# Kernel optimization log

Measured on AMD Instinct MI355X. Metric: run time of the kernel, lower is better.

Reference implementation:

```python
import jax, jax.numpy as jnp
import numpy as np

K = 7          # kernel_size
PAD = K // 2   # padding


def _unfold(t):
    """im2col for kxk neighborhood: (B,C,H,W) -> (B,C,K*K,H,W), zero-padded."""
    B, C, H, W = t.shape
    p = jnp.pad(t, ((0, 0), (0, 0), (PAD, PAD), (PAD, PAD)))
    # row-major over kernel offsets matches F.unfold ordering
    wins = jnp.stack([p[:, :, i:i + H, j:j + W]
                      for i in range(K) for j in range(K)], axis=2)
    return wins


def setup_inputs() -> dict:
    key = jax.random.key(0)
    ks = jax.random.split(key, 7)
    B, C, H, W = 8, 128, 64, 64
    scale = 1.0 / np.sqrt(C)
    x = jax.random.normal(ks[0], (B, C, H, W), dtype=jnp.float32)
    Wq = jax.random.normal(ks[1], (C, C), dtype=jnp.float32) * scale
    Wk = jax.random.normal(ks[2], (C, C), dtype=jnp.float32) * scale
    Wv = jax.random.normal(ks[3], (C, C), dtype=jnp.float32) * scale
    bq = jax.random.normal(ks[4], (C,), dtype=jnp.float32) * 0.01
    bk = jax.random.normal(ks[5], (C,), dtype=jnp.float32) * 0.01
    bv = jax.random.normal(ks[6], (C,), dtype=jnp.float32) * 0.01
    return {"x": x, "Wq": Wq, "bq": bq, "Wk": Wk, "bk": bk, "Wv": Wv, "bv": bv}


def reference(x, Wq, bq, Wk, bk, Wv, bv):
    # 1x1 convs = channel GEMMs
    q = jnp.einsum('oc,bchw->bohw', Wq, x) + bq[:, None, None]
    k = jnp.einsum('oc,bchw->bohw', Wk, x) + bk[:, None, None]
    v = jnp.einsum('oc,bchw->bohw', Wv, x) + bv[:, None, None]
    k_unf = _unfold(k)   # (B,C,K*K,H,W)
    v_unf = _unfold(v)   # (B,C,K*K,H,W)
    # attention scores over the K*K neighborhood, summed over channels
    attn = jnp.einsum('bchw,bcphw->bphw', q, k_unf)
    attn = jax.nn.softmax(attn, axis=1)
    y = jnp.einsum('bphw,bcphw->bchw', attn, v_unf)
    return y
```

## Files before the change

### kernel.cpp

```cpp
#include <hip/hip_runtime.h>
#include <hip/hip_bf16.h>

#define CC   128
#define HH_  64
#define WW_  64
#define BB   8
#define HWSZ (HH_*WW_)
#define CHW  (CC*HWSZ)
#define BCHW (BB*CHW)
#define PAD  3
#define NP   49

typedef __attribute__((ext_vector_type(8))) short short8;
typedef __attribute__((ext_vector_type(4))) float float4v;

__global__ __launch_bounds__(256) void prep_w(
    const float* __restrict__ Wq, const float* __restrict__ Wk,
    const float* __restrict__ Wv,
    unsigned short* __restrict__ whi, unsigned short* __restrict__ wlo)
{
    int i = blockIdx.x * 256 + threadIdx.x;
    const float* src = (i < 16384) ? Wq : (i < 32768 ? Wk : Wv);
    float f = src[i & 16383];
    __hip_bfloat16 h = __float2bfloat16(f);
    float hf = __bfloat162float(h);
    __hip_bfloat16 l = __float2bfloat16(f - hf);
    unsigned short hu, lu;
    __builtin_memcpy(&hu, &h, 2);
    __builtin_memcpy(&lu, &l, 2);
    whi[i] = hu;
    wlo[i] = lu;
}

__global__ __launch_bounds__(256, 2) void qkv_mfma(
    const float* __restrict__ x,
    const unsigned short* __restrict__ whi, const unsigned short* __restrict__ wlo,
    const float* __restrict__ bq, const float* __restrict__ bk,
    const float* __restrict__ bv, float* __restrict__ qkv)
{
    __shared__ unsigned short xT[2][128][136];
    const int proj = blockIdx.y;
    const int n0g  = blockIdx.x << 7;
    const int b    = n0g >> 12;
    const int npx  = n0g & 4095;
    const int tid  = threadIdx.x;
    const int lane = tid & 63;
    const int wv   = tid >> 6;
    const int wm   = wv & 1, wn = wv >> 1;

    const float* xb = x + (size_t)b*CHW + npx;
    #pragma unroll
    for (int it = 0; it < 16; ++it) {
        int f  = tid + (it << 8);
        int c  = f >> 5;
        int p4 = (f & 31) << 2;
        float4 v = *(const float4*)&xb[(size_t)c*HWSZ + p4];
        float vv[4] = {v.x, v.y, v.z, v.w};
        #pragma unroll
        for (int u = 0; u < 4; ++u) {
            __hip_bfloat16 h = __float2bfloat16(vv[u]);
            float hf = __bfloat162float(h);
            __hip_bfloat16 l = __float2bfloat16(vv[u] - hf);
            unsigned short hu, lu;
            __builtin_memcpy(&hu, &h, 2);
            __builtin_memcpy(&lu, &l, 2);
            xT[0][p4 + u][c] = hu;
            xT[1][p4 + u][c] = lu;
        }
    }

    const float* Bp = (proj == 0) ? bq : (proj == 1 ? bk : bv);
    const int q4 = lane >> 4;
    float4v acc[4][4];
    #pragma unroll
    for (int sm = 0; sm < 4; ++sm) {
        const int mb = wm*64 + sm*16 + q4*4;
        float4v bi;
        bi[0] = Bp[mb+0]; bi[1] = Bp[mb+1]; bi[2] = Bp[mb+2]; bi[3] = Bp[mb+3];
        #pragma unroll
        for (int sn = 0; sn < 4; ++sn) acc[sm][sn] = bi;
    }

    __syncthreads();

    const unsigned short* Wh = whi + (size_t)proj*16384;
    const unsigned short* Wl = wlo + (size_t)proj*16384;
    const int kq8  = q4 << 3;
    const int mrow = lane & 15;

    for (int pass = 0; pass < 3; ++pass) {
        const unsigned short* Wp = (pass == 2) ? Wl : Wh;
        const int xi = (pass == 1) ? 1 : 0;
        #pragma unroll
        for (int kc = 0; kc < 4; ++kc) {
            const int kb = kc << 5;
            short8 a[4], bf[4];
            #pragma unroll
            for (int sm = 0; sm < 4; ++sm) {
                const int m = wm*64 + sm*16 + mrow;
                a[sm] = *(const short8*)&Wp[(size_t)m*CC + kb + kq8];
            }
            #pragma unroll
            for (int sn = 0; sn < 4; ++sn) {
                const int n = wn*64 + sn*16 + mrow;
                bf[sn] = *(const short8*)&xT[xi][n][kb + kq8];
            }
            #pragma unroll
            for (int sm = 0; sm < 4; ++sm)
                #pragma unroll
                for (int sn = 0; sn < 4; ++sn)
                    acc[sm][sn] = __builtin_amdgcn_mfma_f32_16x16x32_bf16(
                        a[sm], bf[sn], acc[sm][sn], 0, 0, 0);
        }
    }

    float* op = qkv + (size_t)proj*BCHW + (size_t)b*CHW + npx;
    #pragma unroll
    for (int sm = 0; sm < 4; ++sm) {
        const int mb = wm*64 + sm*16 + q4*4;
        #pragma unroll
        for (int sn = 0; sn < 4; ++sn) {
            const int n = wn*64 + sn*16 + mrow;
            #pragma unroll
            for (int r = 0; r < 4; ++r)
                op[(size_t)(mb + r)*HWSZ + n] = acc[sm][sn][r];
        }
    }
}

__device__ __forceinline__ void load_chunk8(const float* __restrict__ src,
                                            int h0, int c0, float4* stg) {
    const int tid = threadIdx.x;
    #pragma unroll
    for (int i = 0; i < 4; ++i) {
        int f   = tid + (i << 9);
        int c   = f >> 7;
        int rem = f & 127;
        int r   = rem >> 4;
        int q4  = (rem & 15) << 2;
        int hh  = h0 - PAD + r;
        if ((unsigned)hh < (unsigned)HH_)
            stg[i] = *(const float4*)&src[(size_t)(c0 + c)*HWSZ + hh*WW_ + q4];
        else
            stg[i] = make_float4(0.f, 0.f, 0.f, 0.f);
    }
}

__global__ __launch_bounds__(512) void locatt(
    const float* __restrict__ qkv, float* __restrict__ out)
{
    __shared__ __align__(16) float smem[8*72*17];
    __shared__ float lg[2][NP][64];
    __shared__ float dn[2][64];

    const int blk = blockIdx.x;
    const int xs  = blk & 7;
    const int jj  = blk >> 3;
    const int b   = jj >> 2;
    const int h0  = (((xs << 2) | (jj & 3)) << 1);
    const int tid = threadIdx.x;
    const int s   = tid >> 6;
    const int lane = tid & 63;
    const int q16  = lane & 15;
    const int csub = lane >> 4;
    const int w4   = q16 << 2;
    const int w    = lane;

    const float* qp = qkv + (size_t)b*CHW;
    const float* kp = qkv + (size_t)BCHW + (size_t)b*CHW;
    const float* vp = qkv + (size_t)2*BCHW + (size_t)b*CHW;

    float (*ks)[8][72] = (float(*)[8][72])smem;

    if (tid < 256) {
        int idx = tid & 127;
        int c = idx >> 3, r = idx & 7;
        int col = (tid < 128) ? 0 : 68;
        *(float4*)&ks[c][r][col] = make_float4(0.f, 0.f, 0.f, 0.f);
    }

    const bool do0 = (s < 7);
    const bool do1 = (s >= 1);

    float acc0[7][4], acc1[7][4];
    #pragma unroll
    for (int dx = 0; dx < 7; ++dx)
        #pragma unroll
        for (int j = 0; j < 4; ++j) { acc0[dx][j] = 0.f; acc1[dx][j] = 0.f; }

    float4 stg[4];
    load_chunk8(kp, h0, 0, stg);

    for (int ck = 0; ck < 8; ++ck) {
        #pragma unroll
        for (int i = 0; i < 4; ++i) {
            int f   = tid + (i << 9);
            int c   = f >> 7;
            int rem = f & 127;
            int r   = rem >> 4;
            int q4  = (rem & 15) << 2;
            *(float4*)&ks[c][r][4 + q4] = stg[i];
        }
        __syncthreads();
        if (ck < 7) load_chunk8(kp, h0, (ck + 1) * 16, stg);

        const int c0 = ck << 4;
        #pragma unroll
        for (int ci4 = 0; ci4 < 4; ++ci4) {
            const int c = (ci4 << 2) + csub;
            const float* qc = qp + (size_t)(c0 + c)*HWSZ + h0*WW_ + w4;
            float4 q0v = do0 ? *(const float4*)qc
                             : make_float4(0.f, 0.f, 0.f, 0.f);
            float4 q1v = do1 ? *(const float4*)(qc + WW_)
                             : make_float4(0.f, 0.f, 0.f, 0.f);
            float4 ka  = *(const float4*)&ks[c][s][w4];
            float4 kb  = *(const float4*)&ks[c][s][w4 + 4];
            float4 kc2 = *(const float4*)&ks[c][s][w4 + 8];
            float kw[12] = {ka.x,ka.y,ka.z,ka.w, kb.x,kb.y,kb.z,kb.w,
                            kc2.x,kc2.y,kc2.z,kc2.w};
            float q0a[4] = {q0v.x,q0v.y,q0v.z,q0v.w};
            float q1a[4] = {q1v.x,q1v.y,q1v.z,q1v.w};
            #pragma unroll
            for (int dx = 0; dx < 7; ++dx)
                #pragma unroll
                for (int j = 0; j < 4; ++j) {
                    float kv = kw[j + dx + 1];
                    acc0[dx][j] = fmaf(q0a[j], kv, acc0[dx][j]);
                    acc1[dx][j] = fmaf(q1a[j], kv, acc1[dx][j]);
                }
        }
        __syncthreads();
    }

    #pragma unroll
    for (int dx = 0; dx < 7; ++dx)
        #pragma unroll
        for (int j = 0; j < 4; ++j) {
            acc0[dx][j] += __shfl_xor(acc0[dx][j], 16, 64);
            acc0[dx][j] += __shfl_xor(acc0[dx][j], 32, 64);
            acc1[dx][j] += __shfl_xor(acc1[dx][j], 16, 64);
            acc1[dx][j] += __shfl_xor(acc1[dx][j], 32, 64);
        }
    #pragma unroll
    for (int dx = 0; dx < 7; ++dx) {
        if ((dx & 3) == csub) {
            if (do0) *(float4*)&lg[0][s*7 + dx][w4] =
                make_float4(acc0[dx][0], acc0[dx][1], acc0[dx][2], acc0[dx][3]);
            if (do1) *(float4*)&lg[1][(s-1)*7 + dx][w4] =
                make_float4(acc1[dx][0], acc1[dx][1], acc1[dx][2], acc1[dx][3]);
        }
    }

    float vreg[16];
    {
        #pragma unroll
        for (int i = 0; i < 16; ++i) {
            int c  = 2*s + (i >> 3);
            int r  = i & 7;
            int hh = h0 - PAD + r;
            vreg[i] = ((unsigned)hh < (unsigned)HH_)
                      ? vp[(size_t)c*HWSZ + hh*WW_ + w] : 0.f;
        }
    }
    __syncthreads();

    if (tid < 128) {
        const int r = tid >> 6, px = tid & 63;
        float tv[NP];
        float m = -1e30f;
        #pragma unroll
        for (int p = 0; p < NP; ++p) { tv[p] = lg[r][p][px]; m = fmaxf(m, tv[p]); }
        float d = 0.f;
        #pragma unroll
        for (int p = 0; p < NP; ++p) {
            float e = __expf(tv[p] - m);
            d += e;
            lg[r][p][px] = e;
        }
        dn[r][px] = 1.f / d;
    } else {
        int t = tid - 128;
        for (int i = t; i < 1024; i += 384) {
            int r    = i >> 7;
            int rem  = i & 127;
            int colg = rem >> 4;
            int col  = (colg < 4) ? colg : (64 + colg);
            smem[r*1224 + col*17 + (rem & 15)] = 0.f;
        }
    }
    __syncthreads();

    float a0[NP], a1[NP];
    const float sc0 = dn[0][w], sc1 = dn[1][w];
    #pragma unroll
    for (int p = 0; p < NP; ++p) a0[p] = lg[0][p][w] * sc0;
    #pragma unroll
    for (int p = 0; p < NP; ++p) a1[p] = lg[1][p][w] * sc1;

    for (int ck = 0; ck < 8; ++ck) {
        #pragma unroll
        for (int i = 0; i < 16; ++i) {
            int c = 2*s + (i >> 3);
            int r = i & 7;
            smem[r*1224 + (4 + w)*17 + c] = vreg[i];
        }
        __syncthreads();
        if (ck < 7) {
            int c0v = (ck + 1) << 4;
            #pragma unroll
            for (int i = 0; i < 16; ++i) {
                int c  = 2*s + (i >> 3);
                int r  = i & 7;
                int hh = h0 - PAD + r;
                vreg[i] = ((unsigned)hh < (unsigned)HH_)
                          ? vp[(size_t)(c0v + c)*HWSZ + hh*WW_ + w] : 0.f;
            }
        }
        float y0a = 0.f, y0b = 0.f, y1a = 0.f, y1b = 0.f;
        #pragma unroll
        for (int r = 0; r < 8; ++r) {
            const float* vbase = &smem[r*1224 + (1 + w)*17 + 2*s];
            #pragma unroll
            for (int dx = 0; dx < 7; ++dx) {
                float va = vbase[17*dx];
                float vb = vbase[17*dx + 1];
                if (r < 7) {
                    float aw = a0[r*7 + dx];
                    y0a = fmaf(aw, va, y0a); y0b = fmaf(aw, vb, y0b);
                }
                if (r >= 1) {
                    float aw = a1[(r-1)*7 + dx];
                    y1a = fmaf(aw, va, y1a); y1b = fmaf(aw, vb, y1b);
                }
            }
        }
        float* op = out + (size_t)b*CHW + (size_t)(ck*16 + 2*s)*HWSZ
                        + (size_t)h0*WW_ + w;
        op[0]          = y0a;
        op[WW_]        = y1a;
        op[HWSZ]       = y0b;
        op[HWSZ + WW_] = y1b;
        __syncthreads();
    }
}

extern "C" void kernel_launch(void* const* d_in, const int* in_sizes, int n_in,
                              void* d_out, int out_size, void* d_ws, size_t ws_size,
                              hipStream_t stream) {
    const float* x  = (const float*)d_in[0];
    const float* Wq = (const float*)d_in[1];
    const float* bq = (const float*)d_in[2];
    const float* Wk = (const float*)d_in[3];
    const float* bk = (const float*)d_in[4];
    const float* Wv = (const float*)d_in[5];
    const float* bv = (const float*)d_in[6];
    float* out = (float*)d_out;
    float* qkv = (float*)d_ws;

    unsigned short* whi = (unsigned short*)d_out;
    unsigned short* wlo = whi + 3*16384;

    prep_w  <<<192, 256, 0, stream>>>(Wq, Wk, Wv, whi, wlo);
    qkv_mfma<<<dim3(256, 3), 256, 0, stream>>>(x, whi, wlo, bq, bk, bv, qkv);
    locatt  <<<256, 512, 0, stream>>>(qkv, out);
}
```

Baseline: 145.3 us.

## Split local-attention block work across 1024 threads, one output row per wave

Doubles the locatt block to 1024 threads so each wave handles a single output row (rsel) instead of both rows. This halves the per-thread accumulators and attention-weight arrays (a0/a1 become a single a[49]), which cuts register pressure and per-thread FMA work. The staging loads and V-tile writes are repartitioned across the larger block. The tradeoffs are more barrier participants and some idle waves, since 2 of the 16 K-row waves are inactive.

```diff
diff --git a/kernel.cpp b/kernel.cpp
--- a/kernel.cpp
+++ b/kernel.cpp
@@ -128,12 +128,12 @@
     }
 }
 
-__device__ __forceinline__ void load_chunk8(const float* __restrict__ src,
-                                            int h0, int c0, float4* stg) {
+__device__ __forceinline__ void load_chunk16(const float* __restrict__ src,
+                                             int h0, int c0, float4* stg) {
     const int tid = threadIdx.x;
     #pragma unroll
-    for (int i = 0; i < 4; ++i) {
-        int f   = tid + (i << 9);
+    for (int i = 0; i < 2; ++i) {
+        int f   = tid + (i << 10);
         int c   = f >> 7;
         int rem = f & 127;
         int r   = rem >> 4;
@@ -146,7 +146,7 @@
     }
 }
 
-__global__ __launch_bounds__(512) void locatt(
+__global__ __launch_bounds__(1024) void locatt(
     const float* __restrict__ qkv, float* __restrict__ out)
 {
     __shared__ __align__(16) float smem[8*72*17];
@@ -165,6 +165,8 @@
     const int csub = lane >> 4;
     const int w4   = q16 << 2;
     const int w    = lane;
+    const int rsel = s >> 3;
+    const int kr   = s & 7;
 
     const float* qp = qkv + (size_t)b*CHW;
     const float* kp = qkv + (size_t)BCHW + (size_t)b*CHW;
@@ -179,22 +181,21 @@
         *(float4*)&ks[c][r][col] = make_float4(0.f, 0.f, 0.f, 0.f);
     }
 
-    const bool do0 = (s < 7);
-    const bool do1 = (s >= 1);
-
-    float acc0[7][4], acc1[7][4];
+    const bool active = rsel ? (kr >= 1) : (kr < 7);
+
+    float acc[7][4];
     #pragma unroll
     for (int dx = 0; dx < 7; ++dx)
         #pragma unroll
-        for (int j = 0; j < 4; ++j) { acc0[dx][j] = 0.f; acc1[dx][j] = 0.f; }
-
-    float4 stg[4];
-    load_chunk8(kp, h0, 0, stg);
+        for (int j = 0; j < 4; ++j) acc[dx][j] = 0.f;
+
+    float4 stg[2];
+    load_chunk16(kp, h0, 0, stg);
 
     for (int ck = 0; ck < 8; ++ck) {
         #pragma unroll
-        for (int i = 0; i < 4; ++i) {
-            int f   = tid + (i << 9);
+        for (int i = 0; i < 2; ++i) {
+            int f   = tid + (i << 10);
             int c   = f >> 7;
             int rem = f & 127;
             int r   = rem >> 4;
@@ -202,64 +203,62 @@
             *(float4*)&ks[c][r][4 + q4] = stg[i];
         }
         __syncthreads();
-        if (ck < 7) load_chunk8(kp, h0, (ck + 1) * 16, stg);
-
-        const int c0 = ck << 4;
-        #pragma unroll
-        for (int ci4 = 0; ci4 < 4; ++ci4) {
-            const int c = (ci4 << 2) + csub;
-            const float* qc = qp + (size_t)(c0 + c)*HWSZ + h0*WW_ + w4;
-            float4 q0v = do0 ? *(const float4*)qc
-                             : make_float4(0.f, 0.f, 0.f, 0.f);
-            float4 q1v = do1 ? *(const float4*)(qc + WW_)
-                             : make_float4(0.f, 0.f, 0.f, 0.f);
-            float4 ka  = *(const float4*)&ks[c][s][w4];
-            float4 kb  = *(const float4*)&ks[c][s][w4 + 4];
-            float4 kc2 = *(const float4*)&ks[c][s][w4 + 8];
-            float kw[12] = {ka.x,ka.y,ka.z,ka.w, kb.x,kb.y,kb.z,kb.w,
-                            kc2.x,kc2.y,kc2.z,kc2.w};
-            float q0a[4] = {q0v.x,q0v.y,q0v.z,q0v.w};
-            float q1a[4] = {q1v.x,q1v.y,q1v.z,q1v.w};
-            #pragma unroll
-            for (int dx = 0; dx < 7; ++dx)
+        if (ck < 7) load_chunk16(kp, h0, (ck + 1) * 16, stg);
+
+        if (active) {
+            const int c0 = ck << 4;
+            #pragma unroll
+            for (int ci4 = 0; ci4 < 4; ++ci4) {
+                const int c = (ci4 << 2) + csub;
+                const float* qc = qp + (size_t)(c0 + c)*HWSZ
+                                     + (size_t)(h0 + rsel)*WW_ + w4;
+                float4 qv  = *(const float4*)qc;
+                float4 ka  = *(const float4*)&ks[c][kr][w4];
+                float4 kb  = *(const float4*)&ks[c][kr][w4 + 4];
+                float4 kc2 = *(const float4*)&ks[c][kr][w4 + 8];
+                float kw[12] = {ka.x,ka.y,ka.z,ka.w, kb.x,kb.y,kb.z,kb.w,
+                                kc2.x,kc2.y,kc2.z,kc2.w};
+                float qa[4] = {qv.x,qv.y,qv.z,qv.w};
                 #pragma unroll
-                for (int j = 0; j < 4; ++j) {
-                    float kv = kw[j + dx + 1];
-                    acc0[dx][j] = fmaf(q0a[j], kv, acc0[dx][j]);
-                    acc1[dx][j] = fmaf(q1a[j], kv, acc1[dx][j]);
-                }
+                for (int dx = 0; dx < 7; ++dx)
+                    #pragma unroll
+                    for (int j = 0; j < 4; ++j) {
+                        float kv = kw[j + dx + 1];
+                        acc[dx][j] = fmaf(qa[j], kv, acc[dx][j]);
+                    }
+            }
         }
         __syncthreads();
     }
 
-    #pragma unroll
-    for (int dx = 0; dx < 7; ++dx)
-        #pragma unroll
-        for (int j = 0; j < 4; ++j) {
-            acc0[dx][j] += __shfl_xor(acc0[dx][j], 16, 64);
-            acc0[dx][j] += __shfl_xor(acc0[dx][j], 32, 64);
-            acc1[dx][j] += __shfl_xor(acc1[dx][j], 16, 64);
-            acc1[dx][j] += __shfl_xor(acc1[dx][j], 32, 64);
-        }
-    #pragma unroll
-    for (int dx = 0; dx < 7; ++dx) {
-        if ((dx & 3) == csub) {
-            if (do0) *(float4*)&lg[0][s*7 + dx][w4] =
-                make_float4(acc0[dx][0], acc0[dx][1], acc0[dx][2], acc0[dx][3]);
-            if (do1) *(float4*)&lg[1][(s-1)*7 + dx][w4] =
-                make_float4(acc1[dx][0], acc1[dx][1], acc1[dx][2], acc1[dx][3]);
-        }
-    }
-
-    float vreg[16];
+    if (active) {
+        #pragma unroll
+        for (int dx = 0; dx < 7; ++dx)
+            #pragma unroll
+            for (int j = 0; j < 4; ++j) {
+                acc[dx][j] += __shfl_xor(acc[dx][j], 16, 64);
+                acc[dx][j] += __shfl_xor(acc[dx][j], 32, 64);
+            }
+        const int p0 = rsel ? (kr - 1) * 7 : kr * 7;
+        #pragma unroll
+        for (int dx = 0; dx < 7; ++dx) {
+            if ((dx & 3) == csub)
+                *(float4*)&lg[rsel][p0 + dx][w4] =
+                    make_float4(acc[dx][0], acc[dx][1], acc[dx][2], acc[dx][3]);
+        }
+    }
+
+    const int cpl   = (s & 7) << 1;
+    const int rbase = rsel << 2;
+    float vreg[8];
     {
         #pragma unroll
-        for (int i = 0; i < 16; ++i) {
-            int c  = 2*s + (i >> 3);
-            int r  = i & 7;
+        for (int i = 0; i < 8; ++i) {
+            int ch = i >> 2;
+            int r  = rbase + (i & 3);
             int hh = h0 - PAD + r;
             vreg[i] = ((unsigned)hh < (unsigned)HH_)
-                      ? vp[(size_t)c*HWSZ + hh*WW_ + w] : 0.f;
+                      ? vp[(size_t)(cpl + ch)*HWSZ + hh*WW_ + w] : 0.f;
         }
     }
     __syncthreads();
@@ -280,7 +279,7 @@
         dn[r][px] = 1.f / d;
     } else {
         int t = tid - 128;
-        for (int i = t; i < 1024; i += 384) {
+        for (int i = t; i < 1024; i += 896) {
             int r    = i >> 7;
             int rem  = i & 127;
             int colg = rem >> 4;
@@ -290,56 +289,48 @@
     }
     __syncthreads();
 
-    float a0[NP], a1[NP];
-    const float sc0 = dn[0][w], sc1 = dn[1][w];
-    #pragma unroll
-    for (int p = 0; p < NP; ++p) a0[p] = lg[0][p][w] * sc0;
-    #pragma unroll
-    for (int p = 0; p < NP; ++p) a1[p] = lg[1][p][w] * sc1;
+    float a[NP];
+    const float sc = dn[rsel][w];
+    #pragma unroll
+    for (int p = 0; p < NP; ++p) a[p] = lg[rsel][p][w] * sc;
 
     for (int ck = 0; ck < 8; ++ck) {
         #pragma unroll
-        for (int i = 0; i < 16; ++i) {
-            int c = 2*s + (i >> 3);
-            int r = i & 7;
-            smem[r*1224 + (4 + w)*17 + c] = vreg[i];
+        for (int i = 0; i < 8; ++i) {
+            int ch = i >> 2;
+            int r  = rbase + (i & 3);
+            smem[r*1224 + (4 + w)*17 + cpl + ch] = vreg[i];
         }
         __syncthreads();
         if (ck < 7) {
             int c0v = (ck + 1) << 4;
             #pragma unroll
-            for (int i = 0; i < 16; ++i) {
-                int c  = 2*s + (i >> 3);
-                int r  = i & 7;
+            for (int i = 0; i < 8; ++i) {
+                int ch = i >> 2;
+                int r  = rbase + (i & 3);
                 int hh = h0 - PAD + r;
                 vreg[i] = ((unsigned)hh < (unsigned)HH_)
-                          ? vp[(size_t)(c0v + c)*HWSZ + hh*WW_ + w] : 0.f;
-            }
-        }
-        float y0a = 0.f, y0b = 0.f, y1a = 0.f, y1b = 0.f;
-        #pragma unroll
-        for (int r = 0; r < 8; ++r) {
-            const float* vbase = &smem[r*1224 + (1 + w)*17 + 2*s];
+                          ? vp[(size_t)(c0v + cpl + ch)*HWSZ + hh*WW_ + w] : 0.f;
+            }
+        }
+        float ya = 0.f, yb = 0.f;
+        #pragma unroll
+        for (int rl = 0; rl < 7; ++rl) {
+            const int r = rl + rsel;
+            const float* vbase = &smem[r*1224 + (1 + w)*17 + cpl];
             #pragma unroll
             for (int dx = 0; dx < 7; ++dx) {
                 float va = vbase[17*dx];
                 float vb = vbase[17*dx + 1];
-                if (r < 7) {
-                    float aw = a0[r*7 + dx];
-                    y0a = fmaf(aw, va, y0a); y0b = fmaf(aw, vb, y0b);
-                }
-                if (r >= 1) {
-                    float aw = a1[(r-1)*7 + dx];
-                    y1a = fmaf(aw, va, y1a); y1b = fmaf(aw, vb, y1b);
-                }
-            }
-        }
-        float* op = out + (size_t)b*CHW + (size_t)(ck*16 + 2*s)*HWSZ
-                        + (size_t)h0*WW_ + w;
-        op[0]          = y0a;
-        op[WW_]        = y1a;
-        op[HWSZ]       = y0b;
-        op[HWSZ + WW_] = y1b;
+                float aw = a[rl*7 + dx];
+                ya = fmaf(aw, va, ya);
+                yb = fmaf(aw, vb, yb);
+            }
+        }
+        float* op = out + (size_t)b*CHW + (size_t)(ck*16 + cpl)*HWSZ
+                        + (size_t)(h0 + rsel)*WW_ + w;
+        op[0]    = ya;
+        op[HWSZ] = yb;
         __syncthreads();
     }
 }
@@ -362,5 +353,5 @@
 
     prep_w  <<<192, 256, 0, stream>>>(Wq, Wk, Wv, whi, wlo);
     qkv_mfma<<<dim3(256, 3), 256, 0, stream>>>(x, whi, wlo, bq, bk, bv, qkv);
-    locatt  <<<256, 512, 0, stream>>>(qkv, out);
-}
+    locatt  <<<256, 1024, 0, stream>>>(qkv, out);
+}
```

Measured after the change: 149.8 us. 1.03x slower.

## Double-buffer K/V shared tiles to drop a barrier, swizzle xT LDS layout

Applied to the files above, without the earlier changes.

The local-attention kernel now keeps two shared-memory buffers for the K and V chunks, alternating them by chunk parity. This lets it remove the trailing __syncthreads in each chunk loop, so the store of the next chunk no longer waits for every wave to finish reading the current one. Separately, the QKV projection kernel XOR-swizzles the column index of the transposed bf16 x tile to reduce LDS bank conflicts on the short8 reads. The cost is doubled LDS use in locatt (about 78KB plus the logits arrays), which may lower occupancy, and extra padding zeroing for both buffers.

```diff
diff --git a/kernel.cpp b/kernel.cpp
--- a/kernel.cpp
+++ b/kernel.cpp
@@ -54,6 +54,7 @@
         int f  = tid + (it << 8);
         int c  = f >> 5;
         int p4 = (f & 31) << 2;
+        int csw = (((c >> 3) ^ ((p4 >> 3) & 7)) << 3) | (c & 7);
         float4 v = *(const float4*)&xb[(size_t)c*HWSZ + p4];
         float vv[4] = {v.x, v.y, v.z, v.w};
         #pragma unroll
@@ -64,8 +65,8 @@
             unsigned short hu, lu;
             __builtin_memcpy(&hu, &h, 2);
             __builtin_memcpy(&lu, &l, 2);
-            xT[0][p4 + u][c] = hu;
-            xT[1][p4 + u][c] = lu;
+            xT[0][p4 + u][csw] = hu;
+            xT[1][p4 + u][csw] = lu;
         }
     }
 
@@ -103,7 +104,8 @@
             #pragma unroll
             for (int sn = 0; sn < 4; ++sn) {
                 const int n = wn*64 + sn*16 + mrow;
-                bf[sn] = *(const short8*)&xT[xi][n][kb + kq8];
+                const int scol = (kb + kq8) ^ (((n >> 3) & 7) << 3);
+                bf[sn] = *(const short8*)&xT[xi][n][scol];
             }
             #pragma unroll
             for (int sm = 0; sm < 4; ++sm)
@@ -149,7 +151,7 @@
 __global__ __launch_bounds__(512) void locatt(
     const float* __restrict__ qkv, float* __restrict__ out)
 {
-    __shared__ __align__(16) float smem[8*72*17];
+    __shared__ __align__(16) float smem[2*9792];
     __shared__ float lg[2][NP][64];
     __shared__ float dn[2][64];
 
@@ -170,13 +172,14 @@
     const float* kp = qkv + (size_t)BCHW + (size_t)b*CHW;
     const float* vp = qkv + (size_t)2*BCHW + (size_t)b*CHW;
 
-    float (*ks)[8][72] = (float(*)[8][72])smem;
-
-    if (tid < 256) {
-        int idx = tid & 127;
+    {
+        int buf = tid >> 8;
+        int t2  = tid & 255;
+        int idx = t2 & 127;
         int c = idx >> 3, r = idx & 7;
-        int col = (tid < 128) ? 0 : 68;
-        *(float4*)&ks[c][r][col] = make_float4(0.f, 0.f, 0.f, 0.f);
+        int col = (t2 < 128) ? 0 : 68;
+        *(float4*)&smem[buf*9216 + (c*8 + r)*72 + col] =
+            make_float4(0.f, 0.f, 0.f, 0.f);
     }
 
     const bool do0 = (s < 7);
@@ -192,6 +195,7 @@
     load_chunk8(kp, h0, 0, stg);
 
     for (int ck = 0; ck < 8; ++ck) {
+        float* ksb = smem + (ck & 1)*9216;
         #pragma unroll
         for (int i = 0; i < 4; ++i) {
             int f   = tid + (i << 9);
@@ -199,7 +203,7 @@
             int rem = f & 127;
             int r   = rem >> 4;
             int q4  = (rem & 15) << 2;
-            *(float4*)&ks[c][r][4 + q4] = stg[i];
+            *(float4*)&ksb[(c*8 + r)*72 + 4 + q4] = stg[i];
         }
         __syncthreads();
         if (ck < 7) load_chunk8(kp, h0, (ck + 1) * 16, stg);
@@ -213,9 +217,10 @@
                              : make_float4(0.f, 0.f, 0.f, 0.f);
             float4 q1v = do1 ? *(const float4*)(qc + WW_)
                              : make_float4(0.f, 0.f, 0.f, 0.f);
-            float4 ka  = *(const float4*)&ks[c][s][w4];
-            float4 kb  = *(const float4*)&ks[c][s][w4 + 4];
-            float4 kc2 = *(const float4*)&ks[c][s][w4 + 8];
+            const float* krow = &ksb[(c*8 + s)*72];
+            float4 ka  = *(const float4*)&krow[w4];
+            float4 kb  = *(const float4*)&krow[w4 + 4];
+            float4 kc2 = *(const float4*)&krow[w4 + 8];
             float kw[12] = {ka.x,ka.y,ka.z,ka.w, kb.x,kb.y,kb.z,kb.w,
                             kc2.x,kc2.y,kc2.z,kc2.w};
             float q0a[4] = {q0v.x,q0v.y,q0v.z,q0v.w};
@@ -229,7 +234,6 @@
                     acc1[dx][j] = fmaf(q1a[j], kv, acc1[dx][j]);
                 }
         }
-        __syncthreads();
     }
 
     #pragma unroll
@@ -280,12 +284,14 @@
         dn[r][px] = 1.f / d;
     } else {
         int t = tid - 128;
-        for (int i = t; i < 1024; i += 384) {
-            int r    = i >> 7;
-            int rem  = i & 127;
+        for (int i = t; i < 2048; i += 384) {
+            int buf  = i >> 10;
+            int rem1 = i & 1023;
+            int r    = rem1 >> 7;
+            int rem  = rem1 & 127;
             int colg = rem >> 4;
             int col  = (colg < 4) ? colg : (64 + colg);
-            smem[r*1224 + col*17 + (rem & 15)] = 0.f;
+            smem[buf*9792 + r*1224 + col*17 + (rem & 15)] = 0.f;
         }
     }
     __syncthreads();
@@ -298,11 +304,12 @@
     for (int p = 0; p < NP; ++p) a1[p] = lg[1][p][w] * sc1;
 
     for (int ck = 0; ck < 8; ++ck) {
+        float* vb = smem + (ck & 1)*9792;
         #pragma unroll
         for (int i = 0; i < 16; ++i) {
             int c = 2*s + (i >> 3);
             int r = i & 7;
-            smem[r*1224 + (4 + w)*17 + c] = vreg[i];
+            vb[r*1224 + (4 + w)*17 + c] = vreg[i];
         }
         __syncthreads();
         if (ck < 7) {
@@ -319,18 +326,18 @@
         float y0a = 0.f, y0b = 0.f, y1a = 0.f, y1b = 0.f;
         #pragma unroll
         for (int r = 0; r < 8; ++r) {
-            const float* vbase = &smem[r*1224 + (1 + w)*17 + 2*s];
+            const float* vbase = &vb[r*1224 + (1 + w)*17 + 2*s];
             #pragma unroll
             for (int dx = 0; dx < 7; ++dx) {
                 float va = vbase[17*dx];
-                float vb = vbase[17*dx + 1];
+                float vb2 = vbase[17*dx + 1];
                 if (r < 7) {
                     float aw = a0[r*7 + dx];
-                    y0a = fmaf(aw, va, y0a); y0b = fmaf(aw, vb, y0b);
+                    y0a = fmaf(aw, va, y0a); y0b = fmaf(aw, vb2, y0b);
                 }
                 if (r >= 1) {
                     float aw = a1[(r-1)*7 + dx];
-                    y1a = fmaf(aw, va, y1a); y1b = fmaf(aw, vb, y1b);
+                    y1a = fmaf(aw, va, y1a); y1b = fmaf(aw, vb2, y1b);
                 }
             }
         }
@@ -340,7 +347,6 @@
         op[WW_]        = y1a;
         op[HWSZ]       = y0b;
         op[HWSZ + WW_] = y1b;
-        __syncthreads();
     }
 }
 
```

Result: faster. 136.7 us (-5.9%).
